# Performance work log

Measured on AMD Instinct MI355X. Metric: run time of the kernel, lower is better.

## Reference

```python
import jax, jax.numpy as jnp
import numpy as np

N = 100000      # nodes
E = 1600000     # edges
NFEAT = 128
OUTF = 64
D1 = 64
D2 = 32
ALPHA = 0.2     # LeakyReLU negative slope


def setup_inputs() -> dict:
    key = jax.random.key(0)
    ks = jax.random.split(key, 12)

    def lin(k, fan_in, fan_out):
        s = 1.0 / np.sqrt(fan_in)
        kw, kb = jax.random.split(k)
        W = jax.random.uniform(kw, (fan_in, fan_out), jnp.float32, -s, s)
        b = jax.random.uniform(kb, (fan_out,), jnp.float32, -s, s)
        return W, b

    x = jax.random.normal(ks[0], (N, NFEAT), jnp.float32)
    edge_index = jax.random.randint(ks[1], (2, E), 0, N, jnp.int32)
    adj = jnp.zeros((1,), jnp.int32)  # unused by the module's forward

    W0, b0 = lin(ks[2], NFEAT, OUTF)      # self.linear
    W1, b1 = lin(ks[3], OUTF, D1)         # conv1 weight/bias
    W2, b2 = lin(ks[4], D1, D2)           # conv2 weight/bias
    W3, b3 = lin(ks[5], D2, 1)            # self.linear_2

    return {"x": x, "adj": adj, "edge_index": edge_index,
            "W0": W0, "b0": b0, "W1": W1, "b1": b1,
            "W2": W2, "b2": b2, "W3": W3, "b3": b3}


def gcn_conv(x, W, b, src, dst, n):
    """PyG GCNConv: x@W, add self-loops, sym deg-normalized scatter-add, +bias."""
    h = x @ W                                        # [n, d_out]
    loop = jnp.arange(n, dtype=src.dtype)
    s = jnp.concatenate([src, loop])                 # [E+n]
    d = jnp.concatenate([dst, loop])                 # [E+n]
    deg = jax.ops.segment_sum(jnp.ones_like(d, dtype=h.dtype), d, num_segments=n)
    dis = jnp.where(deg > 0, jax.lax.rsqrt(deg), 0.0)
    norm = dis[s] * dis[d]                           # [E+n]
    msg = h[s] * norm[:, None]                       # gather + scale
    out = jax.ops.segment_sum(msg, d, num_segments=n)
    return out + b


def reference(x, adj, edge_index, W0, b0, W1, b1, W2, b2, W3, b3):
    src, dst = edge_index[0], edge_index[1]
    # dropout layers are identity in eval mode
    h = jax.nn.leaky_relu(x @ W0 + b0, negative_slope=ALPHA)
    h = jax.nn.relu(gcn_conv(h, W1, b1, src, dst, N))
    h = jax.nn.relu(gcn_conv(h, W2, b2, src, dst, N))
    return h @ W3 + b3                               # [N, 1]
```

## Files before the change

kernel.cpp:

```cpp
#include <hip/hip_runtime.h>
#include <hip/hip_bf16.h>

#define NFEAT 128
#define ALPHA 0.2f
#define CBSH 10
#define CB   1024
#define NBMAX 128
#define TILE 4096

__device__ inline unsigned int packbf2(float a, float b) {
  unsigned int ua = __float_as_uint(a), ub = __float_as_uint(b);
  ua = (ua + 0x7fffu + ((ua >> 16) & 1u)) >> 16;
  ub = (ub + 0x7fffu + ((ub >> 16) & 1u)) >> 16;
  return ua | (ub << 16);
}
__device__ inline void unpackbf2(unsigned int u, float& lo, float& hi) {
  lo = __uint_as_float(u << 16);
  hi = __uint_as_float(u & 0xffff0000u);
}


__global__ __launch_bounds__(256) void k_bhist(const int* __restrict__ dst, int* __restrict__ bcnt,
                                               int E, int nbuk) {
  __shared__ int lh[NBMAX];
  int t = threadIdx.x;
  if (t < NBMAX) lh[t] = 0;
  __syncthreads();
  int stride = gridDim.x * 256;
  int E4 = E >> 2;
  const int4* d4 = (const int4*)dst;
  for (int e = blockIdx.x * 256 + t; e < E4; e += stride) {
    int4 v = d4[e];
    atomicAdd(&lh[v.x >> CBSH], 1);
    atomicAdd(&lh[v.y >> CBSH], 1);
    atomicAdd(&lh[v.z >> CBSH], 1);
    atomicAdd(&lh[v.w >> CBSH], 1);
  }
  for (int e = (E4 << 2) + blockIdx.x * 256 + t; e < E; e += stride)
    atomicAdd(&lh[dst[e] >> CBSH], 1);
  __syncthreads();
  if (t < nbuk && lh[t]) atomicAdd(&bcnt[t], lh[t]);
}

__global__ __launch_bounds__(NBMAX) void k_bscan(const int* __restrict__ bcnt, int* __restrict__ brow,
                                                 int* __restrict__ bfill, int nbuk, int E) {
  __shared__ int sc[NBMAX];
  int t = threadIdx.x;
  int v = (t < nbuk) ? bcnt[t] : 0;
  sc[t] = v;
  __syncthreads();
  for (int o = 1; o < NBMAX; o <<= 1) {
    int u = (t >= o) ? sc[t - o] : 0;
    __syncthreads();
    sc[t] += u;
    __syncthreads();
  }
  int ex = sc[t] - v;
  if (t < nbuk) { brow[t] = ex; bfill[t] = ex; }
  if (t == 0) brow[nbuk] = E;
}

__global__ __launch_bounds__(256) void k_bpart(const int* __restrict__ src, const int* __restrict__ dst,
    int* __restrict__ bfill, unsigned int* __restrict__ pairs, int E) {
  __shared__ unsigned long long sp[TILE];
  __shared__ int lh[NBMAX], lo[NBMAX], gb[NBMAX], lf[NBMAX];
  int t = threadIdx.x;
  int tb = blockIdx.x * TILE;
  int cnt = E - tb; if (cnt > TILE) cnt = TILE;
  if (t < NBMAX) { lh[t] = 0; lf[t] = 0; }
  __syncthreads();
  int es[TILE / 256], ed[TILE / 256];
  #pragma unroll
  for (int k = 0; k < TILE / 256; ++k) {
    int li = k * 256 + t;
    bool v = li < cnt;
    es[k] = v ? src[tb + li] : 0;
    ed[k] = v ? dst[tb + li] : -1;
    if (v) atomicAdd(&lh[ed[k] >> CBSH], 1);
  }
  __syncthreads();
  if (t < NBMAX) lo[t] = lh[t];
  __syncthreads();
  for (int o = 1; o < NBMAX; o <<= 1) {
    int u = (t < NBMAX && t >= o) ? lo[t - o] : 0;
    __syncthreads();
    if (t < NBMAX) lo[t] += u;
    __syncthreads();
  }
  if (t < NBMAX) {
    lo[t] -= lh[t];
    if (lh[t] > 0) gb[t] = atomicAdd(&bfill[t], lh[t]);
  }
  __syncthreads();
  #pragma unroll
  for (int k = 0; k < TILE / 256; ++k) if (ed[k] >= 0) {
    int bb = ed[k] >> CBSH;
    int r = atomicAdd(&lf[bb], 1);
    sp[lo[bb] + r] = ((unsigned long long)(unsigned int)es[k] << 32) | (unsigned int)ed[k];
  }
  __syncthreads();
  for (int i = t; i < cnt; i += 256) {
    unsigned long long p = sp[i];
    unsigned int d = (unsigned int)p;
    unsigned int s = (unsigned int)(p >> 32);
    int bb = d >> CBSH;
    pairs[gb[bb] + (i - lo[bb])] = (s << CBSH) | (d & (CB - 1));
  }
}

__global__ __launch_bounds__(1024) void k_bcsr(const unsigned int* __restrict__ pairs,
    const int* __restrict__ brow, int* __restrict__ rowptr, int* __restrict__ lst,
    float* __restrict__ dis, int n, int E) {
  __shared__ int deg[CB];
  __shared__ int woff[16];
  int b = blockIdx.x, t = threadIdx.x;
  int lane = t & 63, w = t >> 6;
  int beg = brow[b], end = brow[b + 1];
  deg[t] = 0;
  __syncthreads();
  for (int i = beg + t; i < end; i += 1024)
    atomicAdd(&deg[pairs[i] & (CB - 1)], 1);
  __syncthreads();
  int d = deg[t];
  int v = d;
  #pragma unroll
  for (int o = 1; o < 64; o <<= 1) {
    int u = __shfl_up(v, o);
    if (lane >= o) v += u;
  }
  if (lane == 63) woff[w] = v;
  __syncthreads();
  if (w == 0) {
    int orig = (lane < 16) ? woff[lane] : 0;
    int s = orig;
    #pragma unroll
    for (int o = 1; o < 16; o <<= 1) {
      int u = __shfl_up(s, o);
      if (lane >= o) s += u;
    }
    if (lane < 16) woff[lane] = s - orig;
  }
  __syncthreads();
  int pos = beg + (v - d) + woff[w];
  int node = (b << CBSH) + t;
  if (node < n) {
    rowptr[node] = pos;
    dis[node] = rsqrtf((float)(d + 1));
  }
  if (b == 0 && t == 0) rowptr[n] = E;
  deg[t] = pos;
  __syncthreads();
  for (int i = beg + t; i < end; i += 1024) {
    unsigned int u = pairs[i];
    int p = atomicAdd(&deg[u & (CB - 1)], 1);
    lst[p] = (int)(u >> CBSH);
  }
}


template<int K, int OW, bool HAS_BIAS, bool LEAKY, bool SCALE, bool OBF>
__global__ __launch_bounds__(256) void k_gemm(const float* __restrict__ A,
    const float* __restrict__ W, const float* __restrict__ bias,
    const float* __restrict__ dis, void* __restrict__ outv, int n) {
  constexpr int WPC = OW / 16;
  constexpr int RPB = (4 / WPC) * 64;
  int w = threadIdx.x >> 6, lane = threadIdx.x & 63;
  int og = __builtin_amdgcn_readfirstlane((w % WPC) * 16);
  int row = blockIdx.x * RPB + (w / WPC) * 64 + lane;
  bool ok = row < n;
  int rowc = ok ? row : 0;
  float acc[16];
  #pragma unroll
  for (int j = 0; j < 16; ++j) acc[j] = 0.f;
  const float4* a4 = (const float4*)(A + (size_t)rowc * K);
  const float* Wg = W + og;
  #pragma unroll 4
  for (int k4 = 0; k4 < K / 4; ++k4) {
    float4 xv = a4[k4];
    #pragma unroll
    for (int kk = 0; kk < 4; ++kk) {
      const float* wr = Wg + (k4 * 4 + kk) * OW;
      float xk = kk == 0 ? xv.x : kk == 1 ? xv.y : kk == 2 ? xv.z : xv.w;
      #pragma unroll
      for (int j = 0; j < 16; ++j) acc[j] += xk * wr[j];
    }
  }
  float sc = SCALE ? dis[rowc] : 1.f;
  #pragma unroll
  for (int j = 0; j < 16; ++j) {
    float v = acc[j];
    if (HAS_BIAS) v += bias[og + j];
    if (SCALE) v *= sc;
    if (LEAKY) v = v > 0.f ? v : ALPHA * v;
    acc[j] = v;
  }
  if (!ok) return;
  if (OBF) {
    uint4 p0, p1;
    p0.x = packbf2(acc[0], acc[1]);  p0.y = packbf2(acc[2], acc[3]);
    p0.z = packbf2(acc[4], acc[5]);  p0.w = packbf2(acc[6], acc[7]);
    p1.x = packbf2(acc[8], acc[9]);  p1.y = packbf2(acc[10], acc[11]);
    p1.z = packbf2(acc[12], acc[13]); p1.w = packbf2(acc[14], acc[15]);
    uint4* o = (uint4*)((unsigned int*)outv + (((size_t)row * OW + og) >> 1));
    o[0] = p0; o[1] = p1;
  } else {
    float4* o = (float4*)((float*)outv + (size_t)row * OW + og);
    o[0] = float4{acc[0], acc[1], acc[2], acc[3]};
    o[1] = float4{acc[4], acc[5], acc[6], acc[7]};
    o[2] = float4{acc[8], acc[9], acc[10], acc[11]};
    o[3] = float4{acc[12], acc[13], acc[14], acc[15]};
  }
}


__global__ __launch_bounds__(256) void k_agg1(const uint4* __restrict__ g4,
    const float* __restrict__ dis, const float* __restrict__ bias,
    const int* __restrict__ rowptr, const int* __restrict__ lst,
    float* __restrict__ h, int n) {
  int wid = (blockIdx.x * 256 + threadIdx.x) >> 6;
  if (wid >= n) return;
  int lane = threadIdx.x & 63;
  int c = lane & 7, q = lane >> 3;
  float a[8];
  #pragma unroll
  for (int j = 0; j < 8; ++j) a[j] = 0.f;
  if (q == 0) {
    uint4 u = g4[(size_t)wid * 8 + c];
    unpackbf2(u.x, a[0], a[1]); unpackbf2(u.y, a[2], a[3]);
    unpackbf2(u.z, a[4], a[5]); unpackbf2(u.w, a[6], a[7]);
  }
  int beg = rowptr[wid], cnt = rowptr[wid + 1] - beg;
  for (int o = q; o < cnt; o += 32) {
    int s[4]; uint4 u[4];
    #pragma unroll
    for (int k = 0; k < 4; ++k)
      s[k] = (o + 8 * k < cnt) ? lst[beg + o + 8 * k] : -1;
    #pragma unroll
    for (int k = 0; k < 4; ++k)
      u[k] = (s[k] >= 0) ? g4[(size_t)s[k] * 8 + c] : uint4{0u, 0u, 0u, 0u};
    #pragma unroll
    for (int k = 0; k < 4; ++k) {
      float l, hv;
      unpackbf2(u[k].x, l, hv); a[0] += l; a[1] += hv;
      unpackbf2(u[k].y, l, hv); a[2] += l; a[3] += hv;
      unpackbf2(u[k].z, l, hv); a[4] += l; a[5] += hv;
      unpackbf2(u[k].w, l, hv); a[6] += l; a[7] += hv;
    }
  }
  #pragma unroll
  for (int j = 0; j < 8; ++j) {
    a[j] += __shfl_xor(a[j], 32);
    a[j] += __shfl_xor(a[j], 16);
    a[j] += __shfl_xor(a[j], 8);
  }
  if (q == 0) {
    float d = dis[wid];
    float vb[8];
    #pragma unroll
    for (int j = 0; j < 8; ++j) {
      float v = d * a[j] + bias[8 * c + j];
      vb[j] = v > 0.f ? v : 0.f;
    }
    float4* hp = (float4*)(h + (size_t)wid * 64 + 8 * c);
    hp[0] = float4{vb[0], vb[1], vb[2], vb[3]};
    hp[1] = float4{vb[4], vb[5], vb[6], vb[7]};
  }
}

__global__ __launch_bounds__(256) void k_agg2(const uint4* __restrict__ g4,
    const float* __restrict__ dis, const float* __restrict__ bias,
    const float* __restrict__ W3, const float* __restrict__ b3,
    const int* __restrict__ rowptr, const int* __restrict__ lst,
    float* __restrict__ out, int n) {
  int wid = (blockIdx.x * 256 + threadIdx.x) >> 6;
  if (wid >= n) return;
  int lane = threadIdx.x & 63;
  int c = lane & 3, q = lane >> 2;
  float a[8];
  #pragma unroll
  for (int j = 0; j < 8; ++j) a[j] = 0.f;
  if (q == 0) {
    uint4 u = g4[(size_t)wid * 4 + c];
    unpackbf2(u.x, a[0], a[1]); unpackbf2(u.y, a[2], a[3]);
    unpackbf2(u.z, a[4], a[5]); unpackbf2(u.w, a[6], a[7]);
  }
  int beg = rowptr[wid], cnt = rowptr[wid + 1] - beg;
  for (int o = q; o < cnt; o += 32) {
    int s[2]; uint4 u[2];
    #pragma unroll
    for (int k = 0; k < 2; ++k)
      s[k] = (o + 16 * k < cnt) ? lst[beg + o + 16 * k] : -1;
    #pragma unroll
    for (int k = 0; k < 2; ++k)
      u[k] = (s[k] >= 0) ? g4[(size_t)s[k] * 4 + c] : uint4{0u, 0u, 0u, 0u};
    #pragma unroll
    for (int k = 0; k < 2; ++k) {
      float l, hv;
      unpackbf2(u[k].x, l, hv); a[0] += l; a[1] += hv;
      unpackbf2(u[k].y, l, hv); a[2] += l; a[3] += hv;
      unpackbf2(u[k].z, l, hv); a[4] += l; a[5] += hv;
      unpackbf2(u[k].w, l, hv); a[6] += l; a[7] += hv;
    }
  }
  #pragma unroll
  for (int j = 0; j < 8; ++j) {
    a[j] += __shfl_xor(a[j], 32);
    a[j] += __shfl_xor(a[j], 16);
    a[j] += __shfl_xor(a[j], 8);
    a[j] += __shfl_xor(a[j], 4);
  }
  float d = dis[wid];
  float r = 0.f;
  #pragma unroll
  for (int j = 0; j < 8; ++j) {
    float v = d * a[j] + bias[8 * c + j];
    v = v > 0.f ? v : 0.f;
    r += v * W3[8 * c + j];
  }
  r += __shfl_xor(r, 2);
  r += __shfl_xor(r, 1);
  if (lane == 0) out[wid] = r + b3[0];
}


extern "C" void kernel_launch(void* const* d_in, const int* in_sizes, int n_in,
                              void* d_out, int out_size, void* d_ws, size_t ws_size,
                              hipStream_t stream) {
  (void)n_in; (void)out_size; (void)ws_size;
  const float* x  = (const float*)d_in[0];
  const int*   ei = (const int*)d_in[2];
  const float* W0 = (const float*)d_in[3];
  const float* b0 = (const float*)d_in[4];
  const float* W1 = (const float*)d_in[5];
  const float* b1 = (const float*)d_in[6];
  const float* W2 = (const float*)d_in[7];
  const float* b2 = (const float*)d_in[8];
  const float* W3 = (const float*)d_in[9];
  const float* b3 = (const float*)d_in[10];
  float* out = (float*)d_out;
  int N = in_sizes[0] / NFEAT;
  int E = in_sizes[2] / 2;
  const int* src = ei;
  const int* dst = ei + E;
  int nbuk = (N + CB - 1) / CB;

  char* ws = (char*)d_ws;
  size_t off = 0;
  auto alloc = [&](size_t bytes) -> char* {
    char* p = ws + off;
    off += (bytes + 255) & ~(size_t)255;
    return p;
  };
  int*   bcnt  = (int*)alloc((size_t)NBMAX * 4);
  int*   brow  = (int*)alloc((size_t)(NBMAX + 1) * 4);
  int*   bfill = (int*)alloc((size_t)NBMAX * 4);
  int*   rowp  = (int*)alloc((size_t)(N + 1) * 4);
  float* dis   = (float*)alloc((size_t)N * 4);
  unsigned int* pairs = (unsigned int*)alloc((size_t)E * 4);
  int*   lst   = (int*)alloc((size_t)E * 4);
  float* bufA  = (float*)alloc((size_t)N * 64 * 4);
  unsigned int* bufG = (unsigned int*)alloc((size_t)N * 32 * 4);

  hipMemsetAsync(bcnt, 0, (size_t)NBMAX * 4, stream);
  k_bhist<<<512, 256, 0, stream>>>(dst, bcnt, E, nbuk);
  k_bscan<<<1, NBMAX, 0, stream>>>(bcnt, brow, bfill, nbuk, E);
  k_bpart<<<(E + TILE - 1) / TILE, 256, 0, stream>>>(src, dst, bfill, pairs, E);
  k_bcsr<<<nbuk, 1024, 0, stream>>>(pairs, brow, rowp, lst, dis, N, E);

  k_gemm<NFEAT, 64, true, true, false, false><<<(N + 63) / 64, 256, 0, stream>>>(x, W0, b0, nullptr, bufA, N);
  k_gemm<64, 64, false, false, true, true><<<(N + 63) / 64, 256, 0, stream>>>(bufA, W1, nullptr, dis, bufG, N);
  k_agg1<<<(N + 3) / 4, 256, 0, stream>>>((const uint4*)bufG, dis, b1, rowp, lst, bufA, N);
  k_gemm<64, 32, false, false, true, true><<<(N + 127) / 128, 256, 0, stream>>>(bufA, W2, nullptr, dis, bufG, N);
  k_agg2<<<(N + 3) / 4, 256, 0, stream>>>((const uint4*)bufG, dis, b2, W3, b3, rowp, lst, out, N);
}
```

Measured before the change: 212.5 us.

## Fuse CSR build stages with dense GEMMs via block-index role split

Independent work now shares launches: the first GEMM runs in the same grid as the destination histogram, and the second GEMM in the same grid as the bucket partition. The aim is to fill the GPU with dense work while the scatter-heavy stages run, and to cut the launch count. Node degrees are now counted with global atomics in the histogram pass, so the degree scaling is ready before the second GEMM. Buckets shrink to 256 nodes (512 buckets) with 256-thread CSR blocks. The per-edge global atomics on the degree array add contention, and the larger partition histogram and scan add per-block overhead.

```diff
diff --git a/kernel.cpp b/kernel.cpp
--- a/kernel.cpp
+++ b/kernel.cpp
@@ -3,9 +3,9 @@
 
 #define NFEAT 128
 #define ALPHA 0.2f
-#define CBSH 10
-#define CB   1024
-#define NBMAX 128
+#define CBSH 8
+#define CB   256
+#define NBMAX 512
 #define TILE 4096
 
 __device__ inline unsigned int packbf2(float a, float b) {
@@ -20,153 +20,15 @@
 }
 
 
-__global__ __launch_bounds__(256) void k_bhist(const int* __restrict__ dst, int* __restrict__ bcnt,
-                                               int E, int nbuk) {
-  __shared__ int lh[NBMAX];
-  int t = threadIdx.x;
-  if (t < NBMAX) lh[t] = 0;
-  __syncthreads();
-  int stride = gridDim.x * 256;
-  int E4 = E >> 2;
-  const int4* d4 = (const int4*)dst;
-  for (int e = blockIdx.x * 256 + t; e < E4; e += stride) {
-    int4 v = d4[e];
-    atomicAdd(&lh[v.x >> CBSH], 1);
-    atomicAdd(&lh[v.y >> CBSH], 1);
-    atomicAdd(&lh[v.z >> CBSH], 1);
-    atomicAdd(&lh[v.w >> CBSH], 1);
-  }
-  for (int e = (E4 << 2) + blockIdx.x * 256 + t; e < E; e += stride)
-    atomicAdd(&lh[dst[e] >> CBSH], 1);
-  __syncthreads();
-  if (t < nbuk && lh[t]) atomicAdd(&bcnt[t], lh[t]);
-}
-
-__global__ __launch_bounds__(NBMAX) void k_bscan(const int* __restrict__ bcnt, int* __restrict__ brow,
-                                                 int* __restrict__ bfill, int nbuk, int E) {
-  __shared__ int sc[NBMAX];
-  int t = threadIdx.x;
-  int v = (t < nbuk) ? bcnt[t] : 0;
-  sc[t] = v;
-  __syncthreads();
-  for (int o = 1; o < NBMAX; o <<= 1) {
-    int u = (t >= o) ? sc[t - o] : 0;
-    __syncthreads();
-    sc[t] += u;
-    __syncthreads();
-  }
-  int ex = sc[t] - v;
-  if (t < nbuk) { brow[t] = ex; bfill[t] = ex; }
-  if (t == 0) brow[nbuk] = E;
-}
-
-__global__ __launch_bounds__(256) void k_bpart(const int* __restrict__ src, const int* __restrict__ dst,
-    int* __restrict__ bfill, unsigned int* __restrict__ pairs, int E) {
-  __shared__ unsigned long long sp[TILE];
-  __shared__ int lh[NBMAX], lo[NBMAX], gb[NBMAX], lf[NBMAX];
-  int t = threadIdx.x;
-  int tb = blockIdx.x * TILE;
-  int cnt = E - tb; if (cnt > TILE) cnt = TILE;
-  if (t < NBMAX) { lh[t] = 0; lf[t] = 0; }
-  __syncthreads();
-  int es[TILE / 256], ed[TILE / 256];
-  #pragma unroll
-  for (int k = 0; k < TILE / 256; ++k) {
-    int li = k * 256 + t;
-    bool v = li < cnt;
-    es[k] = v ? src[tb + li] : 0;
-    ed[k] = v ? dst[tb + li] : -1;
-    if (v) atomicAdd(&lh[ed[k] >> CBSH], 1);
-  }
-  __syncthreads();
-  if (t < NBMAX) lo[t] = lh[t];
-  __syncthreads();
-  for (int o = 1; o < NBMAX; o <<= 1) {
-    int u = (t < NBMAX && t >= o) ? lo[t - o] : 0;
-    __syncthreads();
-    if (t < NBMAX) lo[t] += u;
-    __syncthreads();
-  }
-  if (t < NBMAX) {
-    lo[t] -= lh[t];
-    if (lh[t] > 0) gb[t] = atomicAdd(&bfill[t], lh[t]);
-  }
-  __syncthreads();
-  #pragma unroll
-  for (int k = 0; k < TILE / 256; ++k) if (ed[k] >= 0) {
-    int bb = ed[k] >> CBSH;
-    int r = atomicAdd(&lf[bb], 1);
-    sp[lo[bb] + r] = ((unsigned long long)(unsigned int)es[k] << 32) | (unsigned int)ed[k];
-  }
-  __syncthreads();
-  for (int i = t; i < cnt; i += 256) {
-    unsigned long long p = sp[i];
-    unsigned int d = (unsigned int)p;
-    unsigned int s = (unsigned int)(p >> 32);
-    int bb = d >> CBSH;
-    pairs[gb[bb] + (i - lo[bb])] = (s << CBSH) | (d & (CB - 1));
-  }
-}
-
-__global__ __launch_bounds__(1024) void k_bcsr(const unsigned int* __restrict__ pairs,
-    const int* __restrict__ brow, int* __restrict__ rowptr, int* __restrict__ lst,
-    float* __restrict__ dis, int n, int E) {
-  __shared__ int deg[CB];
-  __shared__ int woff[16];
-  int b = blockIdx.x, t = threadIdx.x;
-  int lane = t & 63, w = t >> 6;
-  int beg = brow[b], end = brow[b + 1];
-  deg[t] = 0;
-  __syncthreads();
-  for (int i = beg + t; i < end; i += 1024)
-    atomicAdd(&deg[pairs[i] & (CB - 1)], 1);
-  __syncthreads();
-  int d = deg[t];
-  int v = d;
-  #pragma unroll
-  for (int o = 1; o < 64; o <<= 1) {
-    int u = __shfl_up(v, o);
-    if (lane >= o) v += u;
-  }
-  if (lane == 63) woff[w] = v;
-  __syncthreads();
-  if (w == 0) {
-    int orig = (lane < 16) ? woff[lane] : 0;
-    int s = orig;
-    #pragma unroll
-    for (int o = 1; o < 16; o <<= 1) {
-      int u = __shfl_up(s, o);
-      if (lane >= o) s += u;
-    }
-    if (lane < 16) woff[lane] = s - orig;
-  }
-  __syncthreads();
-  int pos = beg + (v - d) + woff[w];
-  int node = (b << CBSH) + t;
-  if (node < n) {
-    rowptr[node] = pos;
-    dis[node] = rsqrtf((float)(d + 1));
-  }
-  if (b == 0 && t == 0) rowptr[n] = E;
-  deg[t] = pos;
-  __syncthreads();
-  for (int i = beg + t; i < end; i += 1024) {
-    unsigned int u = pairs[i];
-    int p = atomicAdd(&deg[u & (CB - 1)], 1);
-    lst[p] = (int)(u >> CBSH);
-  }
-}
-
-
 template<int K, int OW, bool HAS_BIAS, bool LEAKY, bool SCALE, bool OBF>
-__global__ __launch_bounds__(256) void k_gemm(const float* __restrict__ A,
+__device__ __forceinline__ void gemm_body(int bid, const float* __restrict__ A,
     const float* __restrict__ W, const float* __restrict__ bias,
     const float* __restrict__ dis, void* __restrict__ outv, int n) {
   constexpr int WPC = OW / 16;
   constexpr int RPB = (4 / WPC) * 64;
   int w = threadIdx.x >> 6, lane = threadIdx.x & 63;
   int og = __builtin_amdgcn_readfirstlane((w % WPC) * 16);
-  int row = blockIdx.x * RPB + (w / WPC) * 64 + lane;
+  int row = bid * RPB + (w / WPC) * 64 + lane;
   bool ok = row < n;
   int rowc = ok ? row : 0;
   float acc[16];
@@ -210,6 +72,185 @@
     o[2] = float4{acc[8], acc[9], acc[10], acc[11]};
     o[3] = float4{acc[12], acc[13], acc[14], acc[15]};
   }
+}
+
+
+__global__ __launch_bounds__(256) void k_fused1(const float* __restrict__ x,
+    const float* __restrict__ W0, const float* __restrict__ b0, float* __restrict__ h0,
+    const int* __restrict__ dst, int* __restrict__ bcnt, int* __restrict__ ndeg,
+    int E, int nbuk, int n, int G0) {
+  if ((int)blockIdx.x < G0) {
+    gemm_body<NFEAT, 64, true, true, false, false>(blockIdx.x, x, W0, b0, nullptr, h0, n);
+    return;
+  }
+  __shared__ int lh[NBMAX];
+  int t = threadIdx.x;
+  int bid = blockIdx.x - G0;
+  for (int i = t; i < NBMAX; i += 256) lh[i] = 0;
+  __syncthreads();
+  int stride = 512 * 256;
+  int E4 = E >> 2;
+  const int4* d4 = (const int4*)dst;
+  for (int e = bid * 256 + t; e < E4; e += stride) {
+    int4 v = d4[e];
+    atomicAdd(&lh[v.x >> CBSH], 1);
+    atomicAdd(&lh[v.y >> CBSH], 1);
+    atomicAdd(&lh[v.z >> CBSH], 1);
+    atomicAdd(&lh[v.w >> CBSH], 1);
+    atomicAdd(&ndeg[v.x], 1);
+    atomicAdd(&ndeg[v.y], 1);
+    atomicAdd(&ndeg[v.z], 1);
+    atomicAdd(&ndeg[v.w], 1);
+  }
+  for (int e = (E4 << 2) + bid * 256 + t; e < E; e += stride) {
+    int d = dst[e];
+    atomicAdd(&lh[d >> CBSH], 1);
+    atomicAdd(&ndeg[d], 1);
+  }
+  __syncthreads();
+  for (int i = t; i < nbuk; i += 256)
+    if (lh[i]) atomicAdd(&bcnt[i], lh[i]);
+}
+
+
+__global__ __launch_bounds__(NBMAX) void k_scandis(const int* __restrict__ bcnt,
+    int* __restrict__ brow, int* __restrict__ bfill, const int* __restrict__ ndeg,
+    float* __restrict__ dis, int nbuk, int E, int n) {
+  if (blockIdx.x > 0) {
+    int i = ((int)blockIdx.x - 1) * NBMAX + (int)threadIdx.x;
+    if (i < n) dis[i] = rsqrtf((float)(ndeg[i] + 1));
+    return;
+  }
+  __shared__ int sc[NBMAX];
+  int t = threadIdx.x;
+  int v = (t < nbuk) ? bcnt[t] : 0;
+  sc[t] = v;
+  __syncthreads();
+  for (int o = 1; o < NBMAX; o <<= 1) {
+    int u = (t >= o) ? sc[t - o] : 0;
+    __syncthreads();
+    sc[t] += u;
+    __syncthreads();
+  }
+  int ex = sc[t] - v;
+  if (t < nbuk) { brow[t] = ex; bfill[t] = ex; }
+  if (t == 0) brow[nbuk] = E;
+}
+
+
+__global__ __launch_bounds__(256) void k_fused2(const float* __restrict__ h0,
+    const float* __restrict__ W1, const float* __restrict__ dis, unsigned int* __restrict__ g1,
+    const int* __restrict__ src, const int* __restrict__ dst,
+    int* __restrict__ bfill, unsigned int* __restrict__ pairs, int E, int n, int G1) {
+  if ((int)blockIdx.x < G1) {
+    gemm_body<64, 64, false, false, true, true>(blockIdx.x, h0, W1, nullptr, dis, g1, n);
+    return;
+  }
+  extern __shared__ char smem[];
+  unsigned long long* sp = (unsigned long long*)smem;
+  int* lh = (int*)(smem + TILE * 8);
+  int* lo = lh + NBMAX;
+  int* gb = lo + NBMAX;
+  int* lf = gb + NBMAX;
+  int* wsum = lf + NBMAX;
+  int t = threadIdx.x;
+  int bid = blockIdx.x - G1;
+  int tb = bid * TILE;
+  int cnt = E - tb; if (cnt > TILE) cnt = TILE;
+  for (int i = t; i < NBMAX; i += 256) { lh[i] = 0; lf[i] = 0; }
+  __syncthreads();
+  int es[TILE / 256], ed[TILE / 256];
+  #pragma unroll
+  for (int k = 0; k < TILE / 256; ++k) {
+    int li = k * 256 + t;
+    bool v = li < cnt;
+    es[k] = v ? src[tb + li] : 0;
+    ed[k] = v ? dst[tb + li] : -1;
+    if (v) atomicAdd(&lh[ed[k] >> CBSH], 1);
+  }
+  __syncthreads();
+  int s0 = lh[2 * t], s1 = lh[2 * t + 1];
+  int ps = s0 + s1;
+  wsum[t] = ps;
+  __syncthreads();
+  for (int o = 1; o < 256; o <<= 1) {
+    int u = (t >= o) ? wsum[t - o] : 0;
+    __syncthreads();
+    wsum[t] += u;
+    __syncthreads();
+  }
+  int ex = wsum[t] - ps;
+  lo[2 * t] = ex;
+  lo[2 * t + 1] = ex + s0;
+  __syncthreads();
+  for (int i = t; i < NBMAX; i += 256)
+    if (lh[i] > 0) gb[i] = atomicAdd(&bfill[i], lh[i]);
+  __syncthreads();
+  #pragma unroll
+  for (int k = 0; k < TILE / 256; ++k) if (ed[k] >= 0) {
+    int bb = ed[k] >> CBSH;
+    int r = atomicAdd(&lf[bb], 1);
+    sp[lo[bb] + r] = ((unsigned long long)(unsigned int)es[k] << 32) | (unsigned int)ed[k];
+  }
+  __syncthreads();
+  for (int i = t; i < cnt; i += 256) {
+    unsigned long long p = sp[i];
+    unsigned int d = (unsigned int)p;
+    unsigned int s = (unsigned int)(p >> 32);
+    int bb = d >> CBSH;
+    pairs[gb[bb] + (i - lo[bb])] = (s << CBSH) | (d & (CB - 1));
+  }
+}
+
+
+__global__ __launch_bounds__(256) void k_bcsr(const unsigned int* __restrict__ pairs,
+    const int* __restrict__ brow, int* __restrict__ rowptr, int* __restrict__ lst,
+    int n, int E) {
+  __shared__ int deg[CB];
+  __shared__ int woff[4];
+  int b = blockIdx.x, t = threadIdx.x;
+  int lane = t & 63, w = t >> 6;
+  int beg = brow[b], end = brow[b + 1];
+  deg[t] = 0;
+  __syncthreads();
+  for (int i = beg + t; i < end; i += 256)
+    atomicAdd(&deg[pairs[i] & (CB - 1)], 1);
+  __syncthreads();
+  int d = deg[t];
+  int v = d;
+  #pragma unroll
+  for (int o = 1; o < 64; o <<= 1) {
+    int u = __shfl_up(v, o);
+    if (lane >= o) v += u;
+  }
+  if (lane == 63) woff[w] = v;
+  __syncthreads();
+  if (t == 0) {
+    int s = 0;
+    #pragma unroll
+    for (int k = 0; k < 4; ++k) { int x = woff[k]; woff[k] = s; s += x; }
+  }
+  __syncthreads();
+  int pos = beg + (v - d) + woff[w];
+  int node = (b << CBSH) + t;
+  if (node < n) rowptr[node] = pos;
+  if (b == 0 && t == 0) rowptr[n] = E;
+  __syncthreads();
+  deg[t] = pos;
+  __syncthreads();
+  for (int i = beg + t; i < end; i += 256) {
+    unsigned int u = pairs[i];
+    int p = atomicAdd(&deg[u & (CB - 1)], 1);
+    lst[p] = (int)(u >> CBSH);
+  }
+}
+
+
+template<int K, int OW, bool HAS_BIAS, bool LEAKY, bool SCALE, bool OBF>
+__global__ __launch_bounds__(256) void k_gemm(const float* __restrict__ A,
+    const float* __restrict__ W, const float* __restrict__ bias,
+    const float* __restrict__ dis, void* __restrict__ outv, int n) {
+  gemm_body<K, OW, HAS_BIAS, LEAKY, SCALE, OBF>(blockIdx.x, A, W, bias, dis, outv, n);
 }
 
 
@@ -354,6 +395,7 @@
   int*   bcnt  = (int*)alloc((size_t)NBMAX * 4);
   int*   brow  = (int*)alloc((size_t)(NBMAX + 1) * 4);
   int*   bfill = (int*)alloc((size_t)NBMAX * 4);
+  int*   ndeg  = (int*)alloc((size_t)N * 4);
   int*   rowp  = (int*)alloc((size_t)(N + 1) * 4);
   float* dis   = (float*)alloc((size_t)N * 4);
   unsigned int* pairs = (unsigned int*)alloc((size_t)E * 4);
@@ -361,14 +403,17 @@
   float* bufA  = (float*)alloc((size_t)N * 64 * 4);
   unsigned int* bufG = (unsigned int*)alloc((size_t)N * 32 * 4);
 
+  int G0 = (N + 63) / 64;
+  int G1 = (N + 63) / 64;
+  int GB = (E + TILE - 1) / TILE;
+  constexpr int SMEM2 = TILE * 8 + NBMAX * 4 * 4 + 256 * 4;
+
   hipMemsetAsync(bcnt, 0, (size_t)NBMAX * 4, stream);
-  k_bhist<<<512, 256, 0, stream>>>(dst, bcnt, E, nbuk);
-  k_bscan<<<1, NBMAX, 0, stream>>>(bcnt, brow, bfill, nbuk, E);
-  k_bpart<<<(E + TILE - 1) / TILE, 256, 0, stream>>>(src, dst, bfill, pairs, E);
-  k_bcsr<<<nbuk, 1024, 0, stream>>>(pairs, brow, rowp, lst, dis, N, E);
-
-  k_gemm<NFEAT, 64, true, true, false, false><<<(N + 63) / 64, 256, 0, stream>>>(x, W0, b0, nullptr, bufA, N);
-  k_gemm<64, 64, false, false, true, true><<<(N + 63) / 64, 256, 0, stream>>>(bufA, W1, nullptr, dis, bufG, N);
+  hipMemsetAsync(ndeg, 0, (size_t)N * 4, stream);
+  k_fused1<<<G0 + 512, 256, 0, stream>>>(x, W0, b0, bufA, dst, bcnt, ndeg, E, nbuk, N, G0);
+  k_scandis<<<1 + (N + NBMAX - 1) / NBMAX, NBMAX, 0, stream>>>(bcnt, brow, bfill, ndeg, dis, nbuk, E, N);
+  k_fused2<<<G1 + GB, 256, SMEM2, stream>>>(bufA, W1, dis, bufG, src, dst, bfill, pairs, E, N, G1);
+  k_bcsr<<<nbuk, 256, 0, stream>>>(pairs, brow, rowp, lst, N, E);
   k_agg1<<<(N + 3) / 4, 256, 0, stream>>>((const uint4*)bufG, dis, b1, rowp, lst, bufA, N);
   k_gemm<64, 32, false, false, true, true><<<(N + 127) / 128, 256, 0, stream>>>(bufA, W2, nullptr, dis, bufG, N);
   k_agg2<<<(N + 3) / 4, 256, 0, stream>>>((const uint4*)bufG, dis, b2, W3, b3, rowp, lst, out, N);
```

After: 258.1 us. +21.5%, slower.
